# Performance work log

Measured on AMD Instinct MI355X. Metric: run time of the kernel, lower is better.

## Reference

```python
import jax, jax.numpy as jnp
import numpy as np

NUM_HEADS = 4

def setup_inputs() -> dict:
    key = jax.random.key(0)
    ks = jax.random.split(key, 5)
    B, N, C = 2, 4096, 256
    s = 0.02
    return {
        "x": jax.random.normal(ks[0], (B, N, C), dtype=jnp.float32),
        "qkv_w": jax.random.normal(ks[1], (3 * C, C), dtype=jnp.float32) * s,
        "qkv_b": jax.random.normal(ks[2], (3 * C,), dtype=jnp.float32) * s,
        "out_w": jax.random.normal(ks[3], (C, C), dtype=jnp.float32) * s,
        "out_b": jax.random.normal(ks[4], (C,), dtype=jnp.float32) * s,
    }

def reference(x, qkv_w, qkv_b, out_w, out_b):
    # x: [B, N, C]; manual multi-head self-attention (eval mode, dropout off)
    B, N, C = x.shape
    H = NUM_HEADS
    D = C // H
    qkv = x @ qkv_w.T + qkv_b                      # [B, N, 3C]
    qkv = qkv.reshape(B, N, 3, H, D)
    qkv = jnp.transpose(qkv, (2, 0, 3, 1, 4))      # [3, B, H, N, D]
    q, k, v = qkv[0], qkv[1], qkv[2]
    scale = D ** -0.5
    attn = jnp.einsum('bhnd,bhmd->bhnm', q, k) * scale  # [B, H, N, N]
    attn = jax.nn.softmax(attn, axis=-1)
    out = jnp.einsum('bhnm,bhmd->bhnd', attn, v)   # [B, H, N, D]
    out = jnp.transpose(out, (0, 2, 1, 3)).reshape(B, N, C)
    return out @ out_w.T + out_b
```

## Files before the change

kernel.cpp:

```cpp
#include <hip/hip_runtime.h>

typedef __bf16 bf16x8 __attribute__((ext_vector_type(8)));
typedef float f32x4 __attribute__((ext_vector_type(4)));

#define MFMA_BF16(a, b, c) __builtin_amdgcn_mfma_f32_16x16x32_bf16((a), (b), (c), 0, 0, 0)

#define C1 0.18033688f

static __device__ __forceinline__ unsigned short f2bf(float f) {
    unsigned int u = __float_as_uint(f);
    unsigned int r = (u + 0x7fffu + ((u >> 16) & 1u)) >> 16;
    return (unsigned short)r;
}
static __device__ __forceinline__ float bf2f(unsigned short us) {
    return __uint_as_float(((unsigned int)us) << 16);
}
static __device__ __forceinline__ float exp2_hw(float x) {
    float r;
    asm("v_exp_f32 %0, %1" : "=v"(r) : "v"(x));
    return r;
}
static __device__ __forceinline__ unsigned pack_rh(float a, float b) {
    return __byte_perm(__float_as_uint(a) + 0x8000u, __float_as_uint(b) + 0x8000u, 0x7632);
}
static __device__ __forceinline__ void gload16(const void* g, void* l) {
    __builtin_amdgcn_global_load_lds(
        (const __attribute__((address_space(1))) unsigned int*)g,
        (__attribute__((address_space(3))) unsigned int*)l, 16, 0, 0);
}

static __device__ __forceinline__ void conv_seg8(const void* src, unsigned short* dst, int n,
                                                 int lb, bool f32) {
    const int base = lb * 2048 + (int)threadIdx.x * 8;
    if (base < n) {
        if (f32) {
            const float4 u0 = *(const float4*)((const float*)src + base);
            const float4 u1 = *(const float4*)((const float*)src + base + 4);
            uint4 p;
            p.x = pack_rh(u0.x, u0.y);
            p.y = pack_rh(u0.z, u0.w);
            p.z = pack_rh(u1.x, u1.y);
            p.w = pack_rh(u1.z, u1.w);
            *(uint4*)(dst + base) = p;
        } else {
            *(uint4*)(dst + base) = *(const uint4*)((const unsigned short*)src + base);
        }
    }
}

__global__ __launch_bounds__(256) void convert_kernel(
    const void* __restrict__ x, const void* __restrict__ qw, const void* __restrict__ qb,
    const void* __restrict__ ow, const void* __restrict__ ob,
    unsigned short* __restrict__ xb, unsigned short* __restrict__ qwb,
    unsigned short* __restrict__ qbb, unsigned short* __restrict__ owb,
    unsigned short* __restrict__ obb, int* __restrict__ flag) {
    __shared__ int tot;
    if (threadIdx.x == 0) tot = 0;
    __syncthreads();
    {
        unsigned short v = ((const unsigned short*)x)[threadIdx.x];
        int e = (v >> 7) & 0xFF;
        if (e >= 195) atomicAdd(&tot, 1);
    }
    __syncthreads();
    const bool f32 = (tot >= 8);
    if (blockIdx.x == 0 && threadIdx.x == 0) flag[0] = f32 ? 1 : 0;

    const int bid = blockIdx.x;
    if (bid < 1024)       conv_seg8(x,  xb,  2097152, bid,        f32);
    else if (bid < 1120)  conv_seg8(qw, qwb, 196608,  bid - 1024, f32);
    else if (bid < 1121)  conv_seg8(qb, qbb, 768,     bid - 1120, f32);
    else if (bid < 1153)  conv_seg8(ow, owb, 65536,   bid - 1121, f32);
    else                  conv_seg8(ob, obb, 256,     bid - 1153, f32);
}

template <bool QKV>
__global__ __launch_bounds__(256) void gemm_kernel(
    const unsigned short* __restrict__ A, const unsigned short* __restrict__ W,
    const unsigned short* __restrict__ bias, unsigned short* __restrict__ Cb,
    float* __restrict__ Cf, const int* __restrict__ flag,
    unsigned short* __restrict__ Vt, int Nout) {
    constexpr int K = 256;
    __shared__ __align__(16) char sm[16384];

    const int tid = threadIdx.x;
    const int lane = tid & 63;
    const int wv = tid >> 6;
    const int m16 = lane & 15;
    const int quad = lane >> 4;
    const int bm = blockIdx.x * 64;
    const int bn = blockIdx.y * 64;

    int bgo[2], blo[2];
#pragma unroll
    for (int i = 0; i < 2; i++) {
        const int c = wv * 128 + i * 64 + lane;
        const int r = c >> 3, g = (c & 7) ^ (r & 7);
        bgo[i] = r * (K * 2) + g * 16;
        blo[i] = c * 16;
    }
    int bro[4][2];
#pragma unroll
    for (int t = 0; t < 4; t++)
#pragma unroll
        for (int ks = 0; ks < 2; ks++) {
            const int row = t * 16 + m16;
            bro[t][ks] = row * 64 + ((4 * ks + quad) ^ (m16 & 7)) * 8;
        }

    const char* bg = (const char*)(W + (size_t)bn * K);
    const unsigned short* ap = A + (size_t)(bm + wv * 16 + m16) * K + quad * 8;

#pragma unroll
    for (int i = 0; i < 2; i++) gload16(bg + bgo[i], sm + blo[i]);
    bf16x8 a0 = *(const bf16x8*)(ap);
    bf16x8 a1 = *(const bf16x8*)(ap + 32);

    f32x4 acc[4] = {};
#pragma unroll
    for (int kb = 0; kb < 4; kb++) {
        __syncthreads();
        const int cur = kb & 1;
        bf16x8 a0n, a1n;
        if (kb < 3) {
            bg += 128;
            char* Bdst = sm + (cur ^ 1) * 8192;
#pragma unroll
            for (int i = 0; i < 2; i++) gload16(bg + bgo[i], Bdst + blo[i]);
            a0n = *(const bf16x8*)(ap + (kb + 1) * 64);
            a1n = *(const bf16x8*)(ap + (kb + 1) * 64 + 32);
        }
        const unsigned short* Blds = (const unsigned short*)(sm + cur * 8192);
#pragma unroll
        for (int ks = 0; ks < 2; ks++) {
            const bf16x8 a = ks ? a1 : a0;
#pragma unroll
            for (int t = 0; t < 4; t++) {
                const bf16x8 b = *(const bf16x8*)(Blds + bro[t][ks]);
                acc[t] = MFMA_BF16(a, b, acc[t]);
            }
        }
        if (kb < 3) {
            a0 = a0n;
            a1 = a1n;
        }
    }

    if (QKV && bn >= 512) {
        __syncthreads();
        unsigned short* tr = (unsigned short*)sm;
        const int lr = wv * 16 + quad * 4;
#pragma unroll
        for (int t = 0; t < 4; t++) {
            const float bv = bf2f(bias[bn + t * 16 + m16]);
            uint2 w;
            w.x = pack_rh(acc[t][0] + bv, acc[t][1] + bv);
            w.y = pack_rh(acc[t][2] + bv, acc[t][3] + bv);
            *(uint2*)&tr[(t * 16 + m16) * 72 + lr] = w;
        }
        __syncthreads();
        const int d = tid >> 2;
        const int ch = (tid & 3) * 16;
        const uint4 o4a = *(const uint4*)&tr[d * 72 + ch];
        const uint4 o4b = *(const uint4*)&tr[d * 72 + ch + 8];
        const int hh = (bn - 512) >> 6;
        const int bb = bm >> 12, n0 = bm & 4095;
        unsigned short* vdst = &Vt[((size_t)((bb * 4 + hh) * 64 + d)) * 4096 + n0 + ch];
        *(uint4*)(vdst) = o4a;
        *(uint4*)(vdst + 8) = o4b;
        return;
    }

    const bool outf = (!QKV) && (flag != nullptr) && (*flag != 0);
    const int row0 = bm + wv * 16 + quad * 4;
#pragma unroll
    for (int t = 0; t < 4; t++) {
        const int col = bn + t * 16 + m16;
        const float bv = bf2f(bias[col]);
        float v[4];
#pragma unroll
        for (int r = 0; r < 4; r++) v[r] = acc[t][r] + bv;
        if (QKV) {
            const float sc = (col < 256) ? C1 : 1.0f;
#pragma unroll
            for (int r = 0; r < 4; r++)
                Cb[(size_t)(row0 + r) * 768 + col] = f2bf(v[r] * sc);
        } else {
            if (outf) {
#pragma unroll
                for (int r = 0; r < 4; r++) Cf[(size_t)(row0 + r) * Nout + col] = v[r];
            } else {
#pragma unroll
                for (int r = 0; r < 4; r++) Cb[(size_t)(row0 + r) * Nout + col] = f2bf(v[r]);
            }
        }
    }
}

__global__ __launch_bounds__(256) void attn_kernel(
    const unsigned short* __restrict__ qkv, const unsigned short* __restrict__ Vt,
    unsigned short* __restrict__ attn, int iters) {
    const int N = 4096, C3 = 768;
    __shared__ __align__(16) char sm[65536];

    const int tid = threadIdx.x;
    const int lane = tid & 63;
    const int wv = tid >> 6;
    const int m16 = lane & 15;
    const int quad = lane >> 4;

    const int bh = blockIdx.x & 7;
    const int qt = blockIdx.x >> 3;
    const int b = bh >> 2, h = bh & 3;

    bf16x8 qf[4][2];
#pragma unroll
    for (int j = 0; j < 4; j++)
#pragma unroll
        for (int ks = 0; ks < 2; ks++)
            qf[j][ks] = *(const bf16x8*)(qkv + ((size_t)b * N + qt * 64 + j * 16 + m16) * C3 +
                                         h * 64 + ks * 32 + quad * 8);

    uint4 ones_u;
    ones_u.x = ones_u.y = ones_u.z = ones_u.w = 0x3F803F80u;
    const bf16x8 ones = *(const bf16x8*)&ones_u;

    int kgo[4], vgo[4], klo[4], vlo[4];
#pragma unroll
    for (int i = 0; i < 4; i++) {
        const int c = wv * 256 + i * 64 + lane;
        const int r = c >> 3, g = (c & 7) ^ (r & 7);
        kgo[i] = r * 1536 + g * 16;
        klo[i] = c * 16;
        const int d = c >> 4, gg = (c & 15) ^ (d & 15);
        vgo[i] = d * 8192 + gg * 16;
        vlo[i] = c * 16;
    }
    int kro[2][2];
#pragma unroll
    for (int mb = 0; mb < 2; mb++)
#pragma unroll
        for (int ks = 0; ks < 2; ks++) {
            const int row = wv * 32 + mb * 16 + m16;
            kro[mb][ks] = row * 64 + ((4 * ks + quad) ^ (m16 & 7)) * 8;
        }
    int vroA[4];
#pragma unroll
    for (int t = 0; t < 4; t++)
        vroA[t] = (t * 16 + m16) * 128 + (((wv * 4 + (quad >> 1)) ^ m16) * 8) + (quad & 1) * 4;

    const char* kgp = (const char*)(qkv + (size_t)b * N * C3 + 256 + h * 64);
    const char* vgp = (const char*)(Vt + (size_t)bh * 64 * N);

#pragma unroll
    for (int i = 0; i < 4; i++) {
        gload16(kgp + kgo[i], sm + klo[i]);
        gload16(vgp + vgo[i], sm + 32768 + vlo[i]);
    }

    f32x4 o[4][4] = {};
    f32x4 o1[4] = {};

    for (int kt = 0; kt < iters; ++kt) {
        __syncthreads();
        const int cur = kt & 1;
        if (kt + 1 < iters) {
            kgp += 128 * 1536;
            vgp += 256;
            char* Kdst = sm + (cur ^ 1) * 16384;
            char* Vdst = sm + 32768 + (cur ^ 1) * 16384;
#pragma unroll
            for (int i = 0; i < 4; i++) {
                gload16(kgp + kgo[i], Kdst + klo[i]);
                gload16(vgp + vgo[i], Vdst + vlo[i]);
            }
        }
        const unsigned short* Kb = (const unsigned short*)(sm + cur * 16384);
        const unsigned short* Vb = (const unsigned short*)(sm + 32768 + cur * 16384);

        f32x4 s[2][4] = {};
#pragma unroll
        for (int mb = 0; mb < 2; mb++)
#pragma unroll
            for (int ks = 0; ks < 2; ks++) {
                const bf16x8 ka = *(const bf16x8*)(Kb + kro[mb][ks]);
#pragma unroll
                for (int j = 0; j < 4; j++) s[mb][j] = MFMA_BF16(ka, qf[j][ks], s[mb][j]);
            }

        bf16x8 pa[4];
#pragma unroll
        for (int j = 0; j < 4; j++) {
            const float e0 = exp2_hw(s[0][j][0]);
            const float e1 = exp2_hw(s[0][j][1]);
            const float e2 = exp2_hw(s[0][j][2]);
            const float e3 = exp2_hw(s[0][j][3]);
            const float e4 = exp2_hw(s[1][j][0]);
            const float e5 = exp2_hw(s[1][j][1]);
            const float e6 = exp2_hw(s[1][j][2]);
            const float e7 = exp2_hw(s[1][j][3]);
            uint4 pw;
            pw.x = pack_rh(e0, e1);
            pw.y = pack_rh(e2, e3);
            pw.z = pack_rh(e4, e5);
            pw.w = pack_rh(e6, e7);
            pa[j] = *(const bf16x8*)&pw;
        }

#pragma unroll
        for (int j = 0; j < 4; j++) o1[j] = MFMA_BF16(pa[j], ones, o1[j]);
#pragma unroll
        for (int t = 0; t < 4; t++) {
            const uint2 va = *(const uint2*)(Vb + vroA[t]);
            const uint2 vc = *(const uint2*)(Vb + (vroA[t] ^ 16));
            uint4 vv;
            vv.x = va.x;
            vv.y = va.y;
            vv.z = vc.x;
            vv.w = vc.y;
            const bf16x8 vb = *(const bf16x8*)&vv;
#pragma unroll
            for (int j = 0; j < 4; j++) o[j][t] = MFMA_BF16(pa[j], vb, o[j][t]);
        }
    }

    __syncthreads();
    float* Ored = (float*)sm;
    float* lsum = (float*)(sm + 16384);
    if (m16 == 0) {
#pragma unroll
        for (int j = 0; j < 4; j++)
#pragma unroll
            for (int r = 0; r < 4; r++)
                lsum[wv * 64 + j * 16 + quad * 4 + r] = o1[j][r];
    }
    const int row = tid >> 4;
    const int col = (tid & 15) * 4;
#pragma unroll
    for (int j = 0; j < 4; j++) {
#pragma unroll
        for (int t = 0; t < 4; t++)
#pragma unroll
            for (int r = 0; r < 4; r++)
                Ored[(wv * 16 + quad * 4 + r) * 64 + t * 16 + m16] = o[j][t][r];
        __syncthreads();
        f32x4 sum = *(f32x4*)&Ored[row * 64 + col];
        sum += *(f32x4*)&Ored[1024 + row * 64 + col];
        sum += *(f32x4*)&Ored[2048 + row * 64 + col];
        sum += *(f32x4*)&Ored[3072 + row * 64 + col];
        const float lq = lsum[j * 16 + row] + lsum[64 + j * 16 + row] +
                         lsum[128 + j * 16 + row] + lsum[192 + j * 16 + row];
        const int n = qt * 64 + j * 16 + row;
        const float inv = 1.0f / lq;
        uint2 w;
        w.x = pack_rh(sum[0] * inv, sum[1] * inv);
        w.y = pack_rh(sum[2] * inv, sum[3] * inv);
        *(uint2*)&attn[((size_t)b * N + n) * 256 + h * 64 + col] = w;
        __syncthreads();
    }
}

extern "C" void kernel_launch(void* const* d_in, const int* in_sizes, int n_in,
                              void* d_out, int out_size, void* d_ws, size_t ws_size,
                              hipStream_t stream) {
    const int B = 2, N = 4096, H = 4;
    const int M = B * N;

    char* wsb = (char*)d_ws;
    int* flag = (int*)wsb;
    unsigned short* xb      = (unsigned short*)(wsb + 64);
    unsigned short* qwb     = xb + 2097152;
    unsigned short* qbb     = qwb + 196608;
    unsigned short* owb     = qbb + 768;
    unsigned short* obb     = owb + 65536;
    unsigned short* qkv_ws  = obb + 256;
    unsigned short* Vt_ws   = qkv_ws + 6291456;
    unsigned short* attn_ws = Vt_ws + 2097152;

    convert_kernel<<<1154, 256, 0, stream>>>(d_in[0], d_in[1], d_in[2], d_in[3], d_in[4],
                                             xb, qwb, qbb, owb, obb, flag);

    gemm_kernel<true><<<dim3(M / 64, 768 / 64), 256, 0, stream>>>(
        xb, qwb, qbb, qkv_ws, nullptr, nullptr, Vt_ws, 768);

    attn_kernel<<<512, 256, 0, stream>>>(qkv_ws, Vt_ws, attn_ws, 32);

    gemm_kernel<false><<<dim3(M / 64, 256 / 64), 256, 0, stream>>>(
        attn_ws, owb, obb, (unsigned short*)d_out, (float*)d_out, flag, nullptr, 256);
}
```

Measured before the change: 142.3 us.

## Give each wave private K/V LDS slices and replace block barriers with vmcnt waits

Each wave now loads and reads only its own 32-key slice of K and V into a private LDS region, so the per-iteration __syncthreads is removed and ordering relies on per-wave s_waitcnt vmcnt counts. The K load is waited on before QK^T and the V load only before the PV MFMAs, which lets V arrive while the exponentials are computed. s_setprio is raised around the MFMA blocks to favour matrix issue across waves. The V swizzle and LDS read offsets change to fit the per-wave layout. The risk is that correctness depends on the exact counts of outstanding global-to-LDS loads.

```diff
diff --git a/kernel.cpp b/kernel.cpp
--- a/kernel.cpp
+++ b/kernel.cpp
@@ -228,12 +228,12 @@
     int kgo[4], vgo[4], klo[4], vlo[4];
 #pragma unroll
     for (int i = 0; i < 4; i++) {
-        const int c = wv * 256 + i * 64 + lane;
+        const int c = i * 64 + lane;
         const int r = c >> 3, g = (c & 7) ^ (r & 7);
-        kgo[i] = r * 1536 + g * 16;
+        kgo[i] = (wv * 32 + r) * 1536 + g * 16;
         klo[i] = c * 16;
-        const int d = c >> 4, gg = (c & 15) ^ (d & 15);
-        vgo[i] = d * 8192 + gg * 16;
+        const int d = c >> 2, js = c & 3, jg = js ^ ((d >> 2) & 3);
+        vgo[i] = d * 8192 + wv * 64 + jg * 16;
         vlo[i] = c * 16;
     }
     int kro[2][2];
@@ -241,44 +241,53 @@
     for (int mb = 0; mb < 2; mb++)
 #pragma unroll
         for (int ks = 0; ks < 2; ks++) {
-            const int row = wv * 32 + mb * 16 + m16;
+            const int row = mb * 16 + m16;
             kro[mb][ks] = row * 64 + ((4 * ks + quad) ^ (m16 & 7)) * 8;
         }
     int vroA[4];
 #pragma unroll
-    for (int t = 0; t < 4; t++)
-        vroA[t] = (t * 16 + m16) * 128 + (((wv * 4 + (quad >> 1)) ^ m16) * 8) + (quad & 1) * 4;
+    for (int t = 0; t < 4; t++) {
+        const int d = t * 16 + m16;
+        const int c0 = (quad >> 1) ^ ((d >> 2) & 3);
+        vroA[t] = d * 32 + c0 * 8 + (quad & 1) * 4;
+    }
+
+    char* Kreg0 = sm + wv * 8192;
+    char* Vreg0 = sm + 32768 + wv * 8192;
 
     const char* kgp = (const char*)(qkv + (size_t)b * N * C3 + 256 + h * 64);
     const char* vgp = (const char*)(Vt + (size_t)bh * 64 * N);
 
 #pragma unroll
-    for (int i = 0; i < 4; i++) {
-        gload16(kgp + kgo[i], sm + klo[i]);
-        gload16(vgp + vgo[i], sm + 32768 + vlo[i]);
-    }
+    for (int i = 0; i < 4; i++) gload16(kgp + kgo[i], Kreg0 + klo[i]);
+#pragma unroll
+    for (int i = 0; i < 4; i++) gload16(vgp + vgo[i], Vreg0 + vlo[i]);
+    const char* kgn = kgp + 128 * 1536;
+    const char* vgn = vgp + 256;
 
     f32x4 o[4][4] = {};
     f32x4 o1[4] = {};
 
     for (int kt = 0; kt < iters; ++kt) {
-        __syncthreads();
         const int cur = kt & 1;
         if (kt + 1 < iters) {
-            kgp += 128 * 1536;
-            vgp += 256;
-            char* Kdst = sm + (cur ^ 1) * 16384;
-            char* Vdst = sm + 32768 + (cur ^ 1) * 16384;
-#pragma unroll
-            for (int i = 0; i < 4; i++) {
-                gload16(kgp + kgo[i], Kdst + klo[i]);
-                gload16(vgp + vgo[i], Vdst + vlo[i]);
-            }
-        }
-        const unsigned short* Kb = (const unsigned short*)(sm + cur * 16384);
-        const unsigned short* Vb = (const unsigned short*)(sm + 32768 + cur * 16384);
+            char* Kdst = Kreg0 + (cur ^ 1) * 4096;
+            char* Vdst = Vreg0 + (cur ^ 1) * 4096;
+#pragma unroll
+            for (int i = 0; i < 4; i++) gload16(kgn + kgo[i], Kdst + klo[i]);
+#pragma unroll
+            for (int i = 0; i < 4; i++) gload16(vgn + vgo[i], Vdst + vlo[i]);
+            kgn += 128 * 1536;
+            vgn += 256;
+            asm volatile("s_waitcnt vmcnt(12)" ::: "memory");
+        } else {
+            asm volatile("s_waitcnt vmcnt(4)" ::: "memory");
+        }
+        const unsigned short* Kb = (const unsigned short*)(Kreg0 + cur * 4096);
+        const unsigned short* Vb = (const unsigned short*)(Vreg0 + cur * 4096);
 
         f32x4 s[2][4] = {};
+        __builtin_amdgcn_s_setprio(1);
 #pragma unroll
         for (int mb = 0; mb < 2; mb++)
 #pragma unroll
@@ -287,6 +296,7 @@
 #pragma unroll
                 for (int j = 0; j < 4; j++) s[mb][j] = MFMA_BF16(ka, qf[j][ks], s[mb][j]);
             }
+        __builtin_amdgcn_s_setprio(0);
 
         bf16x8 pa[4];
 #pragma unroll
@@ -307,6 +317,13 @@
             pa[j] = *(const bf16x8*)&pw;
         }
 
+        if (kt + 1 < iters) {
+            asm volatile("s_waitcnt vmcnt(8)" ::: "memory");
+        } else {
+            asm volatile("s_waitcnt vmcnt(0)" ::: "memory");
+        }
+
+        __builtin_amdgcn_s_setprio(1);
 #pragma unroll
         for (int j = 0; j < 4; j++) o1[j] = MFMA_BF16(pa[j], ones, o1[j]);
 #pragma unroll
@@ -322,6 +339,7 @@
 #pragma unroll
             for (int j = 0; j < 4; j++) o[j][t] = MFMA_BF16(pa[j], vb, o[j][t]);
         }
+        __builtin_amdgcn_s_setprio(0);
     }
 
     __syncthreads();
```

Measured after the change: 136.0 us. -4.4%, faster.
